# Kernel tuning notes

Measured on AMD Instinct MI355X. Metric: run time of the kernel, lower is better.

The kernel has to match this reference:

```python
import jax, jax.numpy as jnp
import numpy as np

N_NODES = 65536
N_EDGES = 1048576
DIM = 64
N_GRAPHS = 16


def setup_inputs() -> dict:
    key = jax.random.key(0)
    ks = jax.random.split(key, 8)
    node_feats = jax.random.normal(ks[0], (N_NODES, DIM), dtype=jnp.float32)
    edge_index = jax.random.randint(ks[1], (2, N_EDGES), 0, N_NODES, dtype=jnp.int32)
    batch_num_nodes = jnp.full((N_GRAPHS,), N_NODES // N_GRAPHS, dtype=jnp.int32)
    s = 1.0 / np.sqrt(DIM)
    W1 = jax.random.normal(ks[2], (DIM, DIM), dtype=jnp.float32) * s
    W2 = jax.random.normal(ks[3], (DIM, DIM), dtype=jnp.float32) * s
    W3 = jax.random.normal(ks[4], (DIM, DIM), dtype=jnp.float32) * s
    b1 = jnp.zeros((DIM,), jnp.float32)
    b2 = jnp.zeros((DIM,), jnp.float32)
    b3 = jnp.zeros((DIM,), jnp.float32)
    return {"node_feats": node_feats, "edge_index": edge_index,
            "batch_num_nodes": batch_num_nodes,
            "W1": W1, "b1": b1, "W2": W2, "b2": b2, "W3": W3, "b3": b3}


def _graph_conv(x, src, dst, W, b, n_nodes):
    # DGL GraphConv with norm='both': D_out^{-1/2} A^T D_in^{-1/2} style sym norm
    ones = jnp.ones((src.shape[0],), x.dtype)
    deg_out = jnp.clip(jax.ops.segment_sum(ones, src, num_segments=n_nodes), 1.0)
    deg_in = jnp.clip(jax.ops.segment_sum(ones, dst, num_segments=n_nodes), 1.0)
    h = x * jax.lax.rsqrt(deg_out)[:, None]          # [N, d] scale by src out-deg
    agg = jax.ops.segment_sum(h[src], dst, num_segments=n_nodes)  # gather+scatter
    agg = agg * jax.lax.rsqrt(deg_in)[:, None]
    return agg @ W + b


def _unbatch(h, batch_num_nodes):
    # pad each graph's node block to max_num_node -> [B, max_n, d]
    bnn = np.asarray(batch_num_nodes)
    B = bnn.shape[0]
    max_n = int(bnn.max())
    offsets = np.concatenate([[0], np.cumsum(bnn)])
    graph_id = np.repeat(np.arange(B), bnn)                 # [N_total]
    pos = np.arange(int(offsets[-1])) - offsets[graph_id]   # position within graph
    out = jnp.zeros((B, max_n, h.shape[1]), h.dtype)
    return out.at[jnp.asarray(graph_id), jnp.asarray(pos)].set(h)


def reference(node_feats, edge_index, batch_num_nodes, W1, b1, W2, b2, W3, b3):
    src, dst = edge_index[0], edge_index[1]
    n = node_feats.shape[0]
    h = jax.nn.relu(_graph_conv(node_feats, src, dst, W1, b1, n))
    h = jax.nn.relu(_graph_conv(h, src, dst, W2, b2, n))
    h = _graph_conv(h, src, dst, W3, b3, n)
    return _unbatch(h, batch_num_nodes)
```

## Files before the change

### kernel.cpp

```cpp
#include <hip/hip_runtime.h>
#include <hip/hip_fp16.h>


#define N_NODES 65536
#define N_EDGES 1048576
#define DIM 64

#define CHUNKS 256
#define EPC (N_EDGES / CHUNKS)
#define HB 128
#define OH_WORDS 16384

struct alignas(8) h4 { __half2 a, b; };

__global__ void edge_hist(const int* __restrict__ src, const int* __restrict__ dst,
                          int* __restrict__ block_hist, unsigned* __restrict__ partial,
                          uint2* __restrict__ zeroA, uint2* __restrict__ zeroB) {
    __shared__ unsigned h[OH_WORDS];
    __shared__ int bh[2][256];
    int t = threadIdx.x;
    int j = blockIdx.x;
    for (int i = t; i < OH_WORDS; i += 256) h[i] = 0;
    bh[0][t] = 0; bh[1][t] = 0;
    __syncthreads();
    if (j == 0) {
        if (t < 16) zeroA[t] = make_uint2(0u, 0u);
        else if (t < 32) zeroB[t - 16] = make_uint2(0u, 0u);
    }
    int base = j * (2 * EPC);
    for (int i = t; i < 2 * EPC; i += 256) {
        int s = src[base + i];
        int d = dst[base + i];
        atomicAdd(&h[s >> 2], 1u << ((s & 3) * 8));
        atomicAdd(&bh[i >> 12][d >> 8], 1);
    }
    __syncthreads();
    unsigned* dp = partial + (size_t)j * OH_WORDS;
    for (int i = t; i < OH_WORDS; i += 256) dp[i] = h[i];
    block_hist[t * CHUNKS + 2 * j]     = bh[0][t];
    block_hist[t * CHUNKS + 2 * j + 1] = bh[1][t];
}

__global__ void part_scan(const int* __restrict__ bh, int* __restrict__ so) {
    __shared__ int s[1024];
    int t = threadIdx.x;
    const int4* b4 = (const int4*)(bh + t * 64);
    int4 v[16];
    int sum = 0;
    #pragma unroll
    for (int i = 0; i < 16; i++) {
        v[i] = b4[i];
        sum += v[i].x + v[i].y + v[i].z + v[i].w;
    }
    s[t] = sum;
    __syncthreads();
    for (int off = 1; off < 1024; off <<= 1) {
        int u = (t >= off) ? s[t - off] : 0;
        __syncthreads();
        s[t] += u;
        __syncthreads();
    }
    int run = s[t] - sum;
    int* o = so + t * 64;
    #pragma unroll
    for (int i = 0; i < 16; i++) {
        o[4 * i + 0] = run; run += v[i].x;
        o[4 * i + 1] = run; run += v[i].y;
        o[4 * i + 2] = run; run += v[i].z;
        o[4 * i + 3] = run; run += v[i].w;
    }
}

__global__ void part_scatter(const int* __restrict__ src, const int* __restrict__ dst,
                             const int* __restrict__ so, int* __restrict__ bpack) {
    __shared__ int cur[256];
    cur[threadIdx.x] = so[threadIdx.x * CHUNKS + blockIdx.x];
    __syncthreads();
    int base = blockIdx.x * EPC;
    for (int i = threadIdx.x; i < EPC; i += 256) {
        int s = src[base + i];
        int d = dst[base + i];
        int pos = atomicAdd(&cur[d >> 8], 1);
        bpack[pos] = s | ((d & 255) << 16);
    }
}

__global__ void bucket_fused(const int* __restrict__ bpack, const int* __restrict__ so,
                             int* __restrict__ row_start, float* __restrict__ rs_in,
                             unsigned short* __restrict__ csr_src) {
    __shared__ int stage[8192];
    __shared__ int h[256], sc[256], cur[256];
    int b = blockIdx.x;
    int t = threadIdx.x;
    int beg = so[b * CHUNKS];
    int end = (b == 255) ? N_EDGES : so[(b + 1) * CHUNKS];
    int n = end - beg;
    h[t] = 0;
    __syncthreads();
    for (int i = t; i < n; i += 256) {
        int p = bpack[beg + i];
        if (i < 8192) stage[i] = p;
        atomicAdd(&h[(p >> 16) & 255], 1);
    }
    __syncthreads();
    int d = h[t];
    sc[t] = d;
    __syncthreads();
    for (int off = 1; off < 256; off <<= 1) {
        int v = (t >= off) ? sc[t - off] : 0;
        __syncthreads();
        sc[t] += v;
        __syncthreads();
    }
    int rsv = beg + sc[t] - d;
    int node = b * 256 + t;
    row_start[node] = rsv;
    rs_in[node] = rsqrtf(d < 1 ? 1.0f : (float)d);
    if (node == N_NODES - 1) row_start[N_NODES] = N_EDGES;
    cur[t] = rsv;
    __syncthreads();
    for (int i = t; i < n; i += 256) {
        int p = (i < 8192) ? stage[i] : bpack[beg + i];
        int pos = atomicAdd(&cur[(p >> 16) & 255], 1);
        csr_src[pos] = (unsigned short)(p & 0xFFFF);
    }
}

__global__ void oh2p_prescale(const unsigned* __restrict__ partial,
                              float* __restrict__ rs_out,
                              const float4* __restrict__ x4, h4* __restrict__ xs) {
    __shared__ int4 psum[256];
    __shared__ float rsl[256];
    int b = blockIdx.x;
    int t = threadIdx.x;
    {
        int wl = t & 63;
        int q  = t >> 6;
        int w = b * 64 + wl;
        int c0 = 0, c1 = 0, c2 = 0, c3 = 0;
        const unsigned* p = partial + (size_t)(q * (HB / 4)) * OH_WORDS + w;
        #pragma unroll 4
        for (int c = 0; c < HB / 4; c++) {
            unsigned v = p[(size_t)c * OH_WORDS];
            c0 += (int)(v & 255u);
            c1 += (int)((v >> 8) & 255u);
            c2 += (int)((v >> 16) & 255u);
            c3 += (int)(v >> 24);
        }
        psum[t] = make_int4(c0, c1, c2, c3);
    }
    __syncthreads();
    if (t < 64) {
        int4 a = psum[t], b2 = psum[t + 64], c = psum[t + 128], d = psum[t + 192];
        int c0 = a.x + b2.x + c.x + d.x;
        int c1 = a.y + b2.y + c.y + d.y;
        int c2 = a.z + b2.z + c.z + d.z;
        int c3 = a.w + b2.w + c.w + d.w;
        int w = b * 64 + t;
        float4 r = make_float4(rsqrtf(c0 < 1 ? 1.0f : (float)c0),
                               rsqrtf(c1 < 1 ? 1.0f : (float)c1),
                               rsqrtf(c2 < 1 ? 1.0f : (float)c2),
                               rsqrtf(c3 < 1 ? 1.0f : (float)c3));
        ((float4*)rs_out)[w] = r;
        rsl[t * 4 + 0] = r.x; rsl[t * 4 + 1] = r.y;
        rsl[t * 4 + 2] = r.z; rsl[t * 4 + 3] = r.w;
    }
    __syncthreads();
    int rowbase = b * 4096;
    for (int i = t; i < 4096; i += 256) {
        float r = rsl[i >> 4];
        float4 v = x4[rowbase + i];
        h4 o;
        o.a = __float22half2_rn(make_float2(v.x * r, v.y * r));
        o.b = __float22half2_rn(make_float2(v.z * r, v.w * r));
        xs[rowbase + i] = o;
    }
}

template<bool SCALE_OUT>
__global__ void fused_layer(const uint4* __restrict__ xs16, const int* __restrict__ row_start,
                            const unsigned short* __restrict__ csr,
                            const float* __restrict__ rs_out, const float* __restrict__ rs_in,
                            const float* __restrict__ W, const float* __restrict__ b,
                            void* __restrict__ outp) {
    __shared__ float4 Ws4[DIM * 16];
    __shared__ float4 bs4[16];
    {
        const float4* Wg = (const float4*)W;
        for (int i = threadIdx.x; i < DIM * 16; i += blockDim.x) Ws4[i] = Wg[i];
        if (threadIdx.x < 16) bs4[threadIdx.x] = ((const float4*)b)[threadIdx.x];
    }
    __syncthreads();

    int wave_id = threadIdx.x >> 6;
    int lane = threadIdx.x & 63;
    int g = lane >> 3;
    int l = lane & 7;
    int node = blockIdx.x * 32 + wave_id * 8 + g;

    int beg = row_start[node];
    int end = row_start[node + 1];

    float a0 = 0.f, a1 = 0.f, a2 = 0.f, a3 = 0.f,
          a4 = 0.f, a5 = 0.f, a6 = 0.f, a7 = 0.f;
    for (int k = beg; k < end; k += 16) {
        int s[16];
        #pragma unroll
        for (int j = 0; j < 16; j++) {
            int kk = k + j;
            int idx = csr[kk];
            s[j] = (kk < end) ? idx : N_NODES;
        }
        uint4 v[16];
        #pragma unroll
        for (int j = 0; j < 16; j++) v[j] = xs16[s[j] * 8 + l];
        #pragma unroll
        for (int j = 0; j < 16; j++) {
            float2 f0 = __half22float2(*(const __half2*)&v[j].x);
            float2 f1 = __half22float2(*(const __half2*)&v[j].y);
            float2 f2 = __half22float2(*(const __half2*)&v[j].z);
            float2 f3 = __half22float2(*(const __half2*)&v[j].w);
            a0 += f0.x; a1 += f0.y; a2 += f1.x; a3 += f1.y;
            a4 += f2.x; a5 += f2.y; a6 += f3.x; a7 += f3.y;
        }
    }
    float ri = rs_in[node];
    a0 *= ri; a1 *= ri; a2 *= ri; a3 *= ri;
    a4 *= ri; a5 *= ri; a6 *= ri; a7 *= ri;

    float4 o0 = bs4[2 * l];
    float4 o1 = bs4[2 * l + 1];
    int gbase = g << 3;
    #pragma unroll
    for (int m = 0; m < 8; m++) {
        float q0 = __shfl(a0, gbase + m, 64);
        float q1 = __shfl(a1, gbase + m, 64);
        float q2 = __shfl(a2, gbase + m, 64);
        float q3 = __shfl(a3, gbase + m, 64);
        float q4 = __shfl(a4, gbase + m, 64);
        float q5 = __shfl(a5, gbase + m, 64);
        float q6 = __shfl(a6, gbase + m, 64);
        float q7 = __shfl(a7, gbase + m, 64);
        int rb = (8 * m) * 16 + 2 * l;
        float4 w;
        w = Ws4[rb];            o0.x += q0*w.x; o0.y += q0*w.y; o0.z += q0*w.z; o0.w += q0*w.w;
        w = Ws4[rb + 1];        o1.x += q0*w.x; o1.y += q0*w.y; o1.z += q0*w.z; o1.w += q0*w.w;
        w = Ws4[rb + 16];       o0.x += q1*w.x; o0.y += q1*w.y; o0.z += q1*w.z; o0.w += q1*w.w;
        w = Ws4[rb + 17];       o1.x += q1*w.x; o1.y += q1*w.y; o1.z += q1*w.z; o1.w += q1*w.w;
        w = Ws4[rb + 32];       o0.x += q2*w.x; o0.y += q2*w.y; o0.z += q2*w.z; o0.w += q2*w.w;
        w = Ws4[rb + 33];       o1.x += q2*w.x; o1.y += q2*w.y; o1.z += q2*w.z; o1.w += q2*w.w;
        w = Ws4[rb + 48];       o0.x += q3*w.x; o0.y += q3*w.y; o0.z += q3*w.z; o0.w += q3*w.w;
        w = Ws4[rb + 49];       o1.x += q3*w.x; o1.y += q3*w.y; o1.z += q3*w.z; o1.w += q3*w.w;
        w = Ws4[rb + 64];       o0.x += q4*w.x; o0.y += q4*w.y; o0.z += q4*w.z; o0.w += q4*w.w;
        w = Ws4[rb + 65];       o1.x += q4*w.x; o1.y += q4*w.y; o1.z += q4*w.z; o1.w += q4*w.w;
        w = Ws4[rb + 80];       o0.x += q5*w.x; o0.y += q5*w.y; o0.z += q5*w.z; o0.w += q5*w.w;
        w = Ws4[rb + 81];       o1.x += q5*w.x; o1.y += q5*w.y; o1.z += q5*w.z; o1.w += q5*w.w;
        w = Ws4[rb + 96];       o0.x += q6*w.x; o0.y += q6*w.y; o0.z += q6*w.z; o0.w += q6*w.w;
        w = Ws4[rb + 97];       o1.x += q6*w.x; o1.y += q6*w.y; o1.z += q6*w.z; o1.w += q6*w.w;
        w = Ws4[rb + 112];      o0.x += q7*w.x; o0.y += q7*w.y; o0.z += q7*w.z; o0.w += q7*w.w;
        w = Ws4[rb + 113];      o1.x += q7*w.x; o1.y += q7*w.y; o1.z += q7*w.z; o1.w += q7*w.w;
    }
    if (SCALE_OUT) {
        float ro = rs_out[node];
        o0.x = (o0.x < 0.f ? 0.f : o0.x) * ro;
        o0.y = (o0.y < 0.f ? 0.f : o0.y) * ro;
        o0.z = (o0.z < 0.f ? 0.f : o0.z) * ro;
        o0.w = (o0.w < 0.f ? 0.f : o0.w) * ro;
        o1.x = (o1.x < 0.f ? 0.f : o1.x) * ro;
        o1.y = (o1.y < 0.f ? 0.f : o1.y) * ro;
        o1.z = (o1.z < 0.f ? 0.f : o1.z) * ro;
        o1.w = (o1.w < 0.f ? 0.f : o1.w) * ro;
        uint4 ho;
        *(__half2*)&ho.x = __float22half2_rn(make_float2(o0.x, o0.y));
        *(__half2*)&ho.y = __float22half2_rn(make_float2(o0.z, o0.w));
        *(__half2*)&ho.z = __float22half2_rn(make_float2(o1.x, o1.y));
        *(__half2*)&ho.w = __float22half2_rn(make_float2(o1.z, o1.w));
        ((uint4*)outp)[node * 8 + l] = ho;
    } else {
        float4* o4 = (float4*)outp;
        o4[node * 16 + 2 * l]     = o0;
        o4[node * 16 + 2 * l + 1] = o1;
    }
}

extern "C" void kernel_launch(void* const* d_in, const int* in_sizes, int n_in,
                              void* d_out, int out_size, void* d_ws, size_t ws_size,
                              hipStream_t stream) {
    const float* x   = (const float*)d_in[0];
    const int*   ei  = (const int*)d_in[1];
    const int*   src = ei;
    const int*   dst = ei + N_EDGES;
    const float* W1 = (const float*)d_in[3];
    const float* b1 = (const float*)d_in[4];
    const float* W2 = (const float*)d_in[5];
    const float* b2 = (const float*)d_in[6];
    const float* W3 = (const float*)d_in[7];
    const float* b3 = (const float*)d_in[8];
    float* out = (float*)d_out;

    char* ws = (char*)d_ws;
    float* rs        = (float*)ws;
    float* rs_out    = rs;
    float* rs_in     = rs + N_NODES;
    int*   row_start = (int*)(rs + 2 * N_NODES);
    int*   block_h   = row_start + (N_NODES + 256);
    int*   so        = block_h + 256 * CHUNKS;
    unsigned short* csr_src = (unsigned short*)(so + 256 * CHUNKS);
    h4*    bufA      = (h4*)(csr_src + N_EDGES + 16);
    h4*    bufB      = bufA + (size_t)(N_NODES + 1) * 16;
    unsigned* partial = (unsigned*)(bufB + (size_t)(N_NODES + 1) * 16);
    int*   bpack     = (int*)bufB;
    uint2* zeroA     = (uint2*)(bufA + (size_t)N_NODES * 16);
    uint2* zeroB     = (uint2*)(bufB + (size_t)N_NODES * 16);

    const int fb = N_NODES / 32;

    edge_hist    <<<HB, 256, 0, stream>>>(src, dst, block_h, partial, zeroA, zeroB);
    part_scan    <<<1, 1024, 0, stream>>>(block_h, so);
    part_scatter <<<CHUNKS, 256, 0, stream>>>(src, dst, so, bpack);
    bucket_fused <<<256, 256, 0, stream>>>(bpack, so, row_start, rs_in, csr_src);
    oh2p_prescale<<<256, 256, 0, stream>>>(partial, rs_out, (const float4*)x, bufA);

    fused_layer<true ><<<fb, 256, 0, stream>>>((const uint4*)bufA, row_start, csr_src, rs_out, rs_in, W1, b1, (void*)bufB);
    fused_layer<true ><<<fb, 256, 0, stream>>>((const uint4*)bufB, row_start, csr_src, rs_out, rs_in, W2, b2, (void*)bufA);
    fused_layer<false><<<fb, 256, 0, stream>>>((const uint4*)bufA, row_start, csr_src, rs_out, rs_in, W3, b3, (void*)out);
}
```

Baseline: 239.6 us.

## Apply weight before aggregation using MFMA GEMM, simplify aggregation kernel

Reorders each GraphConv layer so the dense transform (x·W) runs first in a separate MFMA-based fp16 GEMM kernel, relying on linearity to commute it with the normalized sum. The aggregation kernel then only gathers pre-transformed rows and adds the bias, removing the per-node shuffle-and-FMA matmul and the shared-memory weight staging. This adds three extra kernel launches and an extra round trip of the intermediate through global memory. It also rounds x·W to fp16 before accumulation, which changes rounding behaviour.

```diff
diff --git a/kernel.cpp b/kernel.cpp
--- a/kernel.cpp
+++ b/kernel.cpp
@@ -12,6 +12,9 @@
 #define OH_WORDS 16384
 
 struct alignas(8) h4 { __half2 a, b; };
+
+typedef _Float16 half8 __attribute__((ext_vector_type(8)));
+typedef float f32x4 __attribute__((ext_vector_type(4)));
 
 __global__ void edge_hist(const int* __restrict__ src, const int* __restrict__ dst,
                           int* __restrict__ block_hist, unsigned* __restrict__ partial,
@@ -177,21 +180,48 @@
     }
 }
 
+__global__ void gemm_xw(const uint4* __restrict__ xs16, const float* __restrict__ W,
+                        __half* __restrict__ P) {
+    int t = threadIdx.x;
+    int wave = t >> 6, l = t & 63;
+    int cl = l & 15, hi = l >> 4;
+    half8 bf[4][2];
+    #pragma unroll
+    for (int ct = 0; ct < 4; ct++)
+        #pragma unroll
+        for (int kt = 0; kt < 2; kt++)
+            #pragma unroll
+            for (int j = 0; j < 8; j++)
+                bf[ct][kt][j] = (_Float16)W[(kt * 32 + hi * 8 + j) * 64 + ct * 16 + cl];
+
+    int row0 = blockIdx.x * 64 + wave * 16;
+    const uint4* arow = xs16 + (size_t)(row0 + cl) * 8;
+    f32x4 acc[4] = {{0.f,0.f,0.f,0.f},{0.f,0.f,0.f,0.f},
+                    {0.f,0.f,0.f,0.f},{0.f,0.f,0.f,0.f}};
+    #pragma unroll
+    for (int kt = 0; kt < 2; kt++) {
+        uint4 raw = arow[kt * 4 + hi];
+        half8 a = *(half8*)&raw;
+        #pragma unroll
+        for (int ct = 0; ct < 4; ct++)
+            acc[ct] = __builtin_amdgcn_mfma_f32_16x16x32_f16(a, bf[ct][kt], acc[ct], 0, 0, 0);
+    }
+    #pragma unroll
+    for (int ct = 0; ct < 4; ct++)
+        #pragma unroll
+        for (int r = 0; r < 4; r++) {
+            int node = row0 + hi * 4 + r;
+            P[(size_t)node * 64 + ct * 16 + cl] = __float2half(acc[ct][r]);
+        }
+    if (blockIdx.x == 0 && t < 16)
+        ((uint2*)(P + (size_t)N_NODES * 64))[t] = make_uint2(0u, 0u);
+}
+
 template<bool SCALE_OUT>
-__global__ void fused_layer(const uint4* __restrict__ xs16, const int* __restrict__ row_start,
-                            const unsigned short* __restrict__ csr,
-                            const float* __restrict__ rs_out, const float* __restrict__ rs_in,
-                            const float* __restrict__ W, const float* __restrict__ b,
-                            void* __restrict__ outp) {
-    __shared__ float4 Ws4[DIM * 16];
-    __shared__ float4 bs4[16];
-    {
-        const float4* Wg = (const float4*)W;
-        for (int i = threadIdx.x; i < DIM * 16; i += blockDim.x) Ws4[i] = Wg[i];
-        if (threadIdx.x < 16) bs4[threadIdx.x] = ((const float4*)b)[threadIdx.x];
-    }
-    __syncthreads();
-
+__global__ void agg_layer(const uint4* __restrict__ P16, const int* __restrict__ row_start,
+                          const unsigned short* __restrict__ csr,
+                          const float* __restrict__ rs_out, const float* __restrict__ rs_in,
+                          const float* __restrict__ b, void* __restrict__ outp) {
     int wave_id = threadIdx.x >> 6;
     int lane = threadIdx.x & 63;
     int g = lane >> 3;
@@ -213,7 +243,7 @@
         }
         uint4 v[16];
         #pragma unroll
-        for (int j = 0; j < 16; j++) v[j] = xs16[s[j] * 8 + l];
+        for (int j = 0; j < 16; j++) v[j] = P16[s[j] * 8 + l];
         #pragma unroll
         for (int j = 0; j < 16; j++) {
             float2 f0 = __half22float2(*(const __half2*)&v[j].x);
@@ -225,41 +255,12 @@
         }
     }
     float ri = rs_in[node];
-    a0 *= ri; a1 *= ri; a2 *= ri; a3 *= ri;
-    a4 *= ri; a5 *= ri; a6 *= ri; a7 *= ri;
-
-    float4 o0 = bs4[2 * l];
-    float4 o1 = bs4[2 * l + 1];
-    int gbase = g << 3;
-    #pragma unroll
-    for (int m = 0; m < 8; m++) {
-        float q0 = __shfl(a0, gbase + m, 64);
-        float q1 = __shfl(a1, gbase + m, 64);
-        float q2 = __shfl(a2, gbase + m, 64);
-        float q3 = __shfl(a3, gbase + m, 64);
-        float q4 = __shfl(a4, gbase + m, 64);
-        float q5 = __shfl(a5, gbase + m, 64);
-        float q6 = __shfl(a6, gbase + m, 64);
-        float q7 = __shfl(a7, gbase + m, 64);
-        int rb = (8 * m) * 16 + 2 * l;
-        float4 w;
-        w = Ws4[rb];            o0.x += q0*w.x; o0.y += q0*w.y; o0.z += q0*w.z; o0.w += q0*w.w;
-        w = Ws4[rb + 1];        o1.x += q0*w.x; o1.y += q0*w.y; o1.z += q0*w.z; o1.w += q0*w.w;
-        w = Ws4[rb + 16];       o0.x += q1*w.x; o0.y += q1*w.y; o0.z += q1*w.z; o0.w += q1*w.w;
-        w = Ws4[rb + 17];       o1.x += q1*w.x; o1.y += q1*w.y; o1.z += q1*w.z; o1.w += q1*w.w;
-        w = Ws4[rb + 32];       o0.x += q2*w.x; o0.y += q2*w.y; o0.z += q2*w.z; o0.w += q2*w.w;
-        w = Ws4[rb + 33];       o1.x += q2*w.x; o1.y += q2*w.y; o1.z += q2*w.z; o1.w += q2*w.w;
-        w = Ws4[rb + 48];       o0.x += q3*w.x; o0.y += q3*w.y; o0.z += q3*w.z; o0.w += q3*w.w;
-        w = Ws4[rb + 49];       o1.x += q3*w.x; o1.y += q3*w.y; o1.z += q3*w.z; o1.w += q3*w.w;
-        w = Ws4[rb + 64];       o0.x += q4*w.x; o0.y += q4*w.y; o0.z += q4*w.z; o0.w += q4*w.w;
-        w = Ws4[rb + 65];       o1.x += q4*w.x; o1.y += q4*w.y; o1.z += q4*w.z; o1.w += q4*w.w;
-        w = Ws4[rb + 80];       o0.x += q5*w.x; o0.y += q5*w.y; o0.z += q5*w.z; o0.w += q5*w.w;
-        w = Ws4[rb + 81];       o1.x += q5*w.x; o1.y += q5*w.y; o1.z += q5*w.z; o1.w += q5*w.w;
-        w = Ws4[rb + 96];       o0.x += q6*w.x; o0.y += q6*w.y; o0.z += q6*w.z; o0.w += q6*w.w;
-        w = Ws4[rb + 97];       o1.x += q6*w.x; o1.y += q6*w.y; o1.z += q6*w.z; o1.w += q6*w.w;
-        w = Ws4[rb + 112];      o0.x += q7*w.x; o0.y += q7*w.y; o0.z += q7*w.z; o0.w += q7*w.w;
-        w = Ws4[rb + 113];      o1.x += q7*w.x; o1.y += q7*w.y; o1.z += q7*w.z; o1.w += q7*w.w;
-    }
+    float4 bb0 = ((const float4*)b)[2 * l];
+    float4 bb1 = ((const float4*)b)[2 * l + 1];
+    float4 o0 = make_float4(a0 * ri + bb0.x, a1 * ri + bb0.y,
+                            a2 * ri + bb0.z, a3 * ri + bb0.w);
+    float4 o1 = make_float4(a4 * ri + bb1.x, a5 * ri + bb1.y,
+                            a6 * ri + bb1.z, a7 * ri + bb1.w);
     if (SCALE_OUT) {
         float ro = rs_out[node];
         o0.x = (o0.x < 0.f ? 0.f : o0.x) * ro;
@@ -309,11 +310,13 @@
     h4*    bufA      = (h4*)(csr_src + N_EDGES + 16);
     h4*    bufB      = bufA + (size_t)(N_NODES + 1) * 16;
     unsigned* partial = (unsigned*)(bufB + (size_t)(N_NODES + 1) * 16);
+    __half* P        = (__half*)partial;
     int*   bpack     = (int*)bufB;
     uint2* zeroA     = (uint2*)(bufA + (size_t)N_NODES * 16);
     uint2* zeroB     = (uint2*)(bufB + (size_t)N_NODES * 16);
 
     const int fb = N_NODES / 32;
+    const int gb = N_NODES / 64;
 
     edge_hist    <<<HB, 256, 0, stream>>>(src, dst, block_h, partial, zeroA, zeroB);
     part_scan    <<<1, 1024, 0, stream>>>(block_h, so);
@@ -321,7 +324,10 @@
     bucket_fused <<<256, 256, 0, stream>>>(bpack, so, row_start, rs_in, csr_src);
     oh2p_prescale<<<256, 256, 0, stream>>>(partial, rs_out, (const float4*)x, bufA);
 
-    fused_layer<true ><<<fb, 256, 0, stream>>>((const uint4*)bufA, row_start, csr_src, rs_out, rs_in, W1, b1, (void*)bufB);
-    fused_layer<true ><<<fb, 256, 0, stream>>>((const uint4*)bufB, row_start, csr_src, rs_out, rs_in, W2, b2, (void*)bufA);
-    fused_layer<false><<<fb, 256, 0, stream>>>((const uint4*)bufA, row_start, csr_src, rs_out, rs_in, W3, b3, (void*)out);
-}
+    gemm_xw  <<<gb, 256, 0, stream>>>((const uint4*)bufA, W1, P);
+    agg_layer<true ><<<fb, 256, 0, stream>>>((const uint4*)P, row_start, csr_src, rs_out, rs_in, b1, (void*)bufB);
+    gemm_xw  <<<gb, 256, 0, stream>>>((const uint4*)bufB, W2, P);
+    agg_layer<true ><<<fb, 256, 0, stream>>>((const uint4*)P, row_start, csr_src, rs_out, rs_in, b2, (void*)bufA);
+    gemm_xw  <<<gb, 256, 0, stream>>>((const uint4*)bufA, W3, P);
+    agg_layer<false><<<fb, 256, 0, stream>>>((const uint4*)P, row_start, csr_src, rs_out, rs_in, b3, (void*)out);
+}
```

New measurement: 254.9 us. +6.4%, slower.

## Replace shared-memory out-degree histograms with global atomics in scatter pass

Applied to the files above, without the earlier changes.

Removes the per-block packed 8-bit shared-memory source-degree histograms and their 8 MB partial-result buffer and reduction pass. Out-degree is now counted with global atomicAdd inside part_scatter, and the prescale kernel reads the degree array directly. hist_dst now only histograms destinations, using one block per chunk. This trades partial-buffer traffic and the reduction for about a million global atomics spread across 65536 addresses.

```diff
diff --git a/kernel.cpp b/kernel.cpp
--- a/kernel.cpp
+++ b/kernel.cpp
@@ -8,37 +8,27 @@
 
 #define CHUNKS 256
 #define EPC (N_EDGES / CHUNKS)
-#define HB 128
-#define OH_WORDS 16384
 
 struct alignas(8) h4 { __half2 a, b; };
 
-__global__ void edge_hist(const int* __restrict__ src, const int* __restrict__ dst,
-                          int* __restrict__ block_hist, unsigned* __restrict__ partial,
-                          uint2* __restrict__ zeroA, uint2* __restrict__ zeroB) {
-    __shared__ unsigned h[OH_WORDS];
-    __shared__ int bh[2][256];
+__global__ void hist_dst(const int* __restrict__ dst, int* __restrict__ block_hist,
+                         int* __restrict__ deg,
+                         uint2* __restrict__ zeroA, uint2* __restrict__ zeroB) {
+    __shared__ int bh[256];
     int t = threadIdx.x;
     int j = blockIdx.x;
-    for (int i = t; i < OH_WORDS; i += 256) h[i] = 0;
-    bh[0][t] = 0; bh[1][t] = 0;
-    __syncthreads();
+    bh[t] = 0;
+    deg[j * 256 + t] = 0;
     if (j == 0) {
         if (t < 16) zeroA[t] = make_uint2(0u, 0u);
         else if (t < 32) zeroB[t - 16] = make_uint2(0u, 0u);
     }
-    int base = j * (2 * EPC);
-    for (int i = t; i < 2 * EPC; i += 256) {
-        int s = src[base + i];
-        int d = dst[base + i];
-        atomicAdd(&h[s >> 2], 1u << ((s & 3) * 8));
-        atomicAdd(&bh[i >> 12][d >> 8], 1);
-    }
-    __syncthreads();
-    unsigned* dp = partial + (size_t)j * OH_WORDS;
-    for (int i = t; i < OH_WORDS; i += 256) dp[i] = h[i];
-    block_hist[t * CHUNKS + 2 * j]     = bh[0][t];
-    block_hist[t * CHUNKS + 2 * j + 1] = bh[1][t];
+    __syncthreads();
+    int base = j * EPC;
+    for (int i = t; i < EPC; i += 256)
+        atomicAdd(&bh[dst[base + i] >> 8], 1);
+    __syncthreads();
+    block_hist[t * CHUNKS + j] = bh[t];
 }
 
 __global__ void part_scan(const int* __restrict__ bh, int* __restrict__ so) {
@@ -72,7 +62,8 @@
 }
 
 __global__ void part_scatter(const int* __restrict__ src, const int* __restrict__ dst,
-                             const int* __restrict__ so, int* __restrict__ bpack) {
+                             const int* __restrict__ so, int* __restrict__ bpack,
+                             int* __restrict__ deg) {
     __shared__ int cur[256];
     cur[threadIdx.x] = so[threadIdx.x * CHUNKS + blockIdx.x];
     __syncthreads();
@@ -82,6 +73,7 @@
         int d = dst[base + i];
         int pos = atomicAdd(&cur[d >> 8], 1);
         bpack[pos] = s | ((d & 255) << 16);
+        atomicAdd(&deg[s], 1);
     }
 }
 
@@ -126,53 +118,25 @@
     }
 }
 
-__global__ void oh2p_prescale(const unsigned* __restrict__ partial,
+__global__ void oh2p_prescale(const int* __restrict__ deg,
                               float* __restrict__ rs_out,
                               const float4* __restrict__ x4, h4* __restrict__ xs) {
-    __shared__ int4 psum[256];
     __shared__ float rsl[256];
     int b = blockIdx.x;
     int t = threadIdx.x;
-    {
-        int wl = t & 63;
-        int q  = t >> 6;
-        int w = b * 64 + wl;
-        int c0 = 0, c1 = 0, c2 = 0, c3 = 0;
-        const unsigned* p = partial + (size_t)(q * (HB / 4)) * OH_WORDS + w;
-        #pragma unroll 4
-        for (int c = 0; c < HB / 4; c++) {
-            unsigned v = p[(size_t)c * OH_WORDS];
-            c0 += (int)(v & 255u);
-            c1 += (int)((v >> 8) & 255u);
-            c2 += (int)((v >> 16) & 255u);
-            c3 += (int)(v >> 24);
-        }
-        psum[t] = make_int4(c0, c1, c2, c3);
-    }
-    __syncthreads();
-    if (t < 64) {
-        int4 a = psum[t], b2 = psum[t + 64], c = psum[t + 128], d = psum[t + 192];
-        int c0 = a.x + b2.x + c.x + d.x;
-        int c1 = a.y + b2.y + c.y + d.y;
-        int c2 = a.z + b2.z + c.z + d.z;
-        int c3 = a.w + b2.w + c.w + d.w;
-        int w = b * 64 + t;
-        float4 r = make_float4(rsqrtf(c0 < 1 ? 1.0f : (float)c0),
-                               rsqrtf(c1 < 1 ? 1.0f : (float)c1),
-                               rsqrtf(c2 < 1 ? 1.0f : (float)c2),
-                               rsqrtf(c3 < 1 ? 1.0f : (float)c3));
-        ((float4*)rs_out)[w] = r;
-        rsl[t * 4 + 0] = r.x; rsl[t * 4 + 1] = r.y;
-        rsl[t * 4 + 2] = r.z; rsl[t * 4 + 3] = r.w;
-    }
+    int node = b * 256 + t;
+    int d = deg[node];
+    float r = rsqrtf(d < 1 ? 1.0f : (float)d);
+    rs_out[node] = r;
+    rsl[t] = r;
     __syncthreads();
     int rowbase = b * 4096;
     for (int i = t; i < 4096; i += 256) {
-        float r = rsl[i >> 4];
+        float r2 = rsl[i >> 4];
         float4 v = x4[rowbase + i];
         h4 o;
-        o.a = __float22half2_rn(make_float2(v.x * r, v.y * r));
-        o.b = __float22half2_rn(make_float2(v.z * r, v.w * r));
+        o.a = __float22half2_rn(make_float2(v.x * r2, v.y * r2));
+        o.b = __float22half2_rn(make_float2(v.z * r2, v.w * r2));
         xs[rowbase + i] = o;
     }
 }
@@ -308,18 +272,18 @@
     unsigned short* csr_src = (unsigned short*)(so + 256 * CHUNKS);
     h4*    bufA      = (h4*)(csr_src + N_EDGES + 16);
     h4*    bufB      = bufA + (size_t)(N_NODES + 1) * 16;
-    unsigned* partial = (unsigned*)(bufB + (size_t)(N_NODES + 1) * 16);
+    int*   deg       = (int*)(bufB + (size_t)(N_NODES + 1) * 16);
     int*   bpack     = (int*)bufB;
     uint2* zeroA     = (uint2*)(bufA + (size_t)N_NODES * 16);
     uint2* zeroB     = (uint2*)(bufB + (size_t)N_NODES * 16);
 
     const int fb = N_NODES / 32;
 
-    edge_hist    <<<HB, 256, 0, stream>>>(src, dst, block_h, partial, zeroA, zeroB);
+    hist_dst     <<<CHUNKS, 256, 0, stream>>>(dst, block_h, deg, zeroA, zeroB);
     part_scan    <<<1, 1024, 0, stream>>>(block_h, so);
-    part_scatter <<<CHUNKS, 256, 0, stream>>>(src, dst, so, bpack);
+    part_scatter <<<CHUNKS, 256, 0, stream>>>(src, dst, so, bpack, deg);
     bucket_fused <<<256, 256, 0, stream>>>(bpack, so, row_start, rs_in, csr_src);
-    oh2p_prescale<<<256, 256, 0, stream>>>(partial, rs_out, (const float4*)x, bufA);
+    oh2p_prescale<<<256, 256, 0, stream>>>(deg, rs_out, (const float4*)x, bufA);
 
     fused_layer<true ><<<fb, 256, 0, stream>>>((const uint4*)bufA, row_start, csr_src, rs_out, rs_in, W1, b1, (void*)bufB);
     fused_layer<true ><<<fb, 256, 0, stream>>>((const uint4*)bufB, row_start, csr_src, rs_out, rs_in, W2, b2, (void*)bufA);
```

Result: slower. 266.6 us (+11.3%).

## Sort edges in shared memory before global writes in partition and bucket kernels

Applied to the files above, without the earlier changes.

The partition scatter kernel now counts each chunk's edges per destination bucket, sorts them locally in LDS by bucket, and writes contiguous runs to global memory. The bucket kernel does the same for the CSR source array, sorting in LDS first and then writing coalesced. Both target the scattered, uncoalesced global writes of the previous atomic-position scheme. In exchange they add LDS usage (a 4096-int plus byte buffer, and an 8192-short buffer), which may lower occupancy, plus an extra prefix scan and barriers.

```diff
diff --git a/kernel.cpp b/kernel.cpp
--- a/kernel.cpp
+++ b/kernel.cpp
@@ -73,15 +73,51 @@
 
 __global__ void part_scatter(const int* __restrict__ src, const int* __restrict__ dst,
                              const int* __restrict__ so, int* __restrict__ bpack) {
-    __shared__ int cur[256];
-    cur[threadIdx.x] = so[threadIdx.x * CHUNKS + blockIdx.x];
-    __syncthreads();
-    int base = blockIdx.x * EPC;
-    for (int i = threadIdx.x; i < EPC; i += 256) {
-        int s = src[base + i];
-        int d = dst[base + i];
-        int pos = atomicAdd(&cur[d >> 8], 1);
-        bpack[pos] = s | ((d & 255) << 16);
+    __shared__ int hist[256], sc[256], off[256], cur[256], gbase[256];
+    __shared__ int sorted[EPC];
+    __shared__ unsigned char pos2b[EPC];
+    int t = threadIdx.x;
+    int j = blockIdx.x;
+    hist[t] = 0;
+    gbase[t] = so[t * CHUNKS + j];
+    __syncthreads();
+    int base = j * EPC;
+    int sv[16], dv[16];
+    #pragma unroll
+    for (int u = 0; u < 16; u++) {
+        int i = base + u * 256 + t;
+        sv[u] = src[i];
+        dv[u] = dst[i];
+        atomicAdd(&hist[dv[u] >> 8], 1);
+    }
+    __syncthreads();
+    int hv = hist[t];
+    sc[t] = hv;
+    __syncthreads();
+    for (int o = 1; o < 256; o <<= 1) {
+        int u = (t >= o) ? sc[t - o] : 0;
+        __syncthreads();
+        sc[t] += u;
+        __syncthreads();
+    }
+    int myoff = sc[t] - hv;
+    off[t] = myoff;
+    cur[t] = myoff;
+    __syncthreads();
+    for (int p = myoff, e = myoff + hv; p < e; p++)
+        pos2b[p] = (unsigned char)t;
+    #pragma unroll
+    for (int u = 0; u < 16; u++) {
+        int b = dv[u] >> 8;
+        int r = atomicAdd(&cur[b], 1);
+        sorted[r] = sv[u] | ((dv[u] & 255) << 16);
+    }
+    __syncthreads();
+    #pragma unroll
+    for (int u = 0; u < 16; u++) {
+        int i = u * 256 + t;
+        int b = pos2b[i];
+        bpack[gbase[b] + (i - off[b])] = sorted[i];
     }
 }
 
@@ -89,6 +125,7 @@
                              int* __restrict__ row_start, float* __restrict__ rs_in,
                              unsigned short* __restrict__ csr_src) {
     __shared__ int stage[8192];
+    __shared__ unsigned short sorted[8192];
     __shared__ int h[256], sc[256], cur[256];
     int b = blockIdx.x;
     int t = threadIdx.x;
@@ -112,17 +149,30 @@
         sc[t] += v;
         __syncthreads();
     }
-    int rsv = beg + sc[t] - d;
+    int excl = sc[t] - d;
     int node = b * 256 + t;
-    row_start[node] = rsv;
+    row_start[node] = beg + excl;
     rs_in[node] = rsqrtf(d < 1 ? 1.0f : (float)d);
     if (node == N_NODES - 1) row_start[N_NODES] = N_EDGES;
-    cur[t] = rsv;
-    __syncthreads();
-    for (int i = t; i < n; i += 256) {
-        int p = (i < 8192) ? stage[i] : bpack[beg + i];
-        int pos = atomicAdd(&cur[(p >> 16) & 255], 1);
-        csr_src[pos] = (unsigned short)(p & 0xFFFF);
+    cur[t] = excl;
+    __syncthreads();
+    if (n <= 8192) {
+        for (int i = t; i < n; i += 256) {
+            int p = stage[i];
+            int r = atomicAdd(&cur[(p >> 16) & 255], 1);
+            sorted[r] = (unsigned short)(p & 0xFFFF);
+        }
+        __syncthreads();
+        for (int i = t; i < n; i += 256)
+            csr_src[beg + i] = sorted[i];
+    } else {
+        cur[t] = beg + excl;
+        __syncthreads();
+        for (int i = t; i < n; i += 256) {
+            int p = (i < 8192) ? stage[i] : bpack[beg + i];
+            int pos = atomicAdd(&cur[(p >> 16) & 255], 1);
+            csr_src[pos] = (unsigned short)(p & 0xFFFF);
+        }
     }
 }
 
```

Result: no change. 236.6 us (-1.2%).
